# Performance work log

Measured on AMD Instinct MI355X. Metric: run time of the kernel, lower is better.

Reference implementation:

```python
import jax, jax.numpy as jnp
import numpy as np

C = 32          # mid_channel / in_channel
B = 8           # batch size (number of scenes)
N = 2_000_000   # total points across batch
BN_EPS = 1e-4   # BatchNorm1d eps from norm_fn


def setup_inputs() -> dict:
    key = jax.random.key(0)
    ks = jax.random.split(key, 8)
    s = 0.05
    return {
        "feats": jax.random.normal(ks[0], (N, C), dtype=jnp.float32),
        "batch_idxs": jnp.sort(jax.random.randint(ks[1], (N,), 0, B, dtype=jnp.int32)),
        "off_w1": jax.random.normal(ks[2], (C, C), dtype=jnp.float32) * s,
        "off_b1": jnp.zeros((C,), jnp.float32),
        "bn_gamma": jnp.ones((C,), jnp.float32),   # set_bn_init fills 1.0
        "bn_beta": jnp.zeros((C,), jnp.float32),   # set_bn_init fills 0.0
        "off_w2": jax.random.normal(ks[3], (C, 3), dtype=jnp.float32) * s,
        "off_b2": jnp.zeros((3,), jnp.float32),
        "mask_w1": jax.random.normal(ks[4], (C, C), dtype=jnp.float32) * s,
        "mask_b1": jnp.zeros((C,), jnp.float32),
        "mask_w2": jax.random.normal(ks[5], (C, 1), dtype=jnp.float32) * s,
        "mask_b2": jnp.zeros((1,), jnp.float32),
        "iou_w": jax.random.normal(ks[6], (C, 1), dtype=jnp.float32) * s,
        "iou_b": jnp.zeros((1,), jnp.float32),
    }


def reference(feats, batch_idxs, off_w1, off_b1, bn_gamma, bn_beta, off_w2, off_b2,
              mask_w1, mask_b1, mask_w2, mask_b2, iou_w, iou_b):
    # offset_linear = MLP([C, C, 3], norm_fn=BatchNorm1d): Linear -> BN -> ReLU -> Linear
    h = feats @ off_w1 + off_b1                      # [N, C]
    mu = h.mean(axis=0)
    var = jnp.mean(jnp.square(h - mu), axis=0)       # biased var (torch BN training fwd)
    h = (h - mu) * jax.lax.rsqrt(var + BN_EPS) * bn_gamma + bn_beta
    h = jax.nn.relu(h)
    pt_offsets = h @ off_w2 + off_b2                 # [N, 3]

    # mask_linear = MLP([C, C, 1], norm_fn=None): Linear -> ReLU -> Linear
    m = jax.nn.relu(feats @ mask_w1 + mask_b1)       # [N, C]
    mask_scores = m @ mask_w2 + mask_b2              # [N, 1]

    # global_pool: scatter mean of features over per-batch segments (batch offsets)
    ones = jnp.ones((feats.shape[0],), feats.dtype)
    counts = jax.ops.segment_sum(ones, batch_idxs, num_segments=B)          # [B]
    pooled = jax.ops.segment_sum(feats, batch_idxs, num_segments=B)         # [B, C]
    pooled = pooled / jnp.maximum(counts, 1.0)[:, None]

    # iou_score_linear on the pooled proposal feature
    iou_scores = pooled @ iou_w + iou_b              # [B, 1]
    return pt_offsets, mask_scores, pooled, iou_scores
```

## Files before the change

kernel.cpp:

```cpp
#include <hip/hip_runtime.h>

#define TPB 256
#define GRID_BLOCKS 1024

typedef __attribute__((ext_vector_type(8))) short short8;
typedef __attribute__((ext_vector_type(4))) float floatx4;

__device__ __forceinline__ unsigned short bf_rne(float f){
    union { float f; unsigned u; } c; c.f = f;
    unsigned r = c.u + 0x7fffu + ((c.u >> 16) & 1u);
    return (unsigned short)(r >> 16);
}
__device__ __forceinline__ unsigned pack_bf(float lo, float hi){
    union { float f; unsigned u; } a, b; a.f = lo; b.f = hi;
    return __builtin_amdgcn_perm(b.u, a.u, 0x07060302u);
}

__global__ __launch_bounds__(TPB, 2) void pass1_kernel(
    const float* __restrict__ feats, const int* __restrict__ bidx,
    const float* __restrict__ w1, const float* __restrict__ b1,
    const float* __restrict__ mw1, const float* __restrict__ mb1,
    const float* __restrict__ mw2, const float* __restrict__ mb2,
    float* __restrict__ mask_out,
    float* __restrict__ ws_sum, float* __restrict__ ws_sq,
    float* __restrict__ ws_pool, int N, int B)
{
    __shared__ float s_pool[8][32];
    __shared__ float s_sum[32];
    __shared__ float s_sq[32];
    __shared__ int   s_lb[9];

    const int tid  = threadIdx.x;
    const int lane = tid & 63;
    const int p = lane & 15;
    const int q = lane >> 4;

    if (tid < 32){ s_sum[tid] = 0.f; s_sq[tid] = 0.f; }
    ((float*)s_pool)[tid] = 0.f;
    if (tid <= B){
        int lo = 0, hi = N;
        while (lo < hi){
            const int mid = (lo + hi) >> 1;
            if (bidx[mid] < tid) lo = mid + 1; else hi = mid;
        }
        s_lb[tid] = lo;
    }
    __syncthreads();

    short8 aw0, aw1, am0, am1;
    floatx4 ci_h0, ci_h1, ci_m0, ci_m1;
    float mw2v[8];
#pragma unroll
    for (int j = 0; j < 8; ++j){
        const int k = q * 8 + j;
        aw0[j] = (short)bf_rne(w1 [k * 32 + p]);
        aw1[j] = (short)bf_rne(w1 [k * 32 + 16 + p]);
        am0[j] = (short)bf_rne(mw1[k * 32 + p]);
        am1[j] = (short)bf_rne(mw1[k * 32 + 16 + p]);
    }
#pragma unroll
    for (int r = 0; r < 4; ++r){
        const int c0 = q * 4 + r, c1 = 16 + q * 4 + r;
        ci_h0[r] = b1[c0];  ci_h1[r] = b1[c1];
        ci_m0[r] = mb1[c0]; ci_m1[r] = mb1[c1];
        mw2v[r] = mw2[c0];  mw2v[4 + r] = mw2[c1];
    }
    const float mb2s = mb2[0];

    float hsum[8] = {0,0,0,0,0,0,0,0};
    float hsq [8] = {0,0,0,0,0,0,0,0};
    float pacc[8] = {0,0,0,0,0,0,0,0};

    const int npairs = (N + 31) >> 5;
    const int nw  = gridDim.x * (TPB / 64);
    const int wid = blockIdx.x * (TPB / 64) + (tid >> 6);
    const int g0  = (int)((long)wid       * npairs / nw);
    const int g1  = (int)((long)(wid + 1) * npairs / nw);

    int curb = 0;
    {
        const int r0 = g0 << 5;
        while (curb < B - 1 && r0 >= s_lb[curb + 1]) curb++;
    }
    int lbn = s_lb[curb + 1];

    const float* rp = feats + (((size_t)g0) << 10) + (p << 5) + (q << 3);

    floatx4 vA0 = {0,0,0,0}, vA1 = {0,0,0,0}, vB0 = {0,0,0,0}, vB1 = {0,0,0,0};
    if (g0 < g1){
        const int rA = (g0 << 5) + p;
        if (rA < N){ const floatx4* vp = (const floatx4*)rp; vA0 = vp[0]; vA1 = vp[1]; }
        if (rA + 16 < N){ const floatx4* vp = (const floatx4*)(rp + 512); vB0 = vp[0]; vB1 = vp[1]; }
    }

    for (int g = g0; g < g1; ++g){
        floatx4 nA0 = {0,0,0,0}, nA1 = {0,0,0,0}, nB0 = {0,0,0,0}, nB1 = {0,0,0,0};
        const float* np = rp + 1024;
        if (g + 1 < g1){
            const int rA = ((g + 1) << 5) + p;
            if (rA < N){ const floatx4* vp = (const floatx4*)np; nA0 = vp[0]; nA1 = vp[1]; }
            if (rA + 16 < N){ const floatx4* vp = (const floatx4*)(np + 512); nB0 = vp[0]; nB1 = vp[1]; }
        }

        const int r0 = g << 5;
        if (r0 >= lbn){
#pragma unroll
            for (int j = 0; j < 8; ++j){
                if (pacc[j] != 0.f) atomicAdd(&s_pool[curb][q * 8 + j], pacc[j]);
                pacc[j] = 0.f;
            }
            do { curb++; } while (curb < B - 1 && r0 >= s_lb[curb + 1]);
            lbn = s_lb[curb + 1];
        }
        const bool slow = (r0 + 31 >= lbn) || (r0 + 31 >= N);

        if (!slow){
            pacc[0] += vA0[0] + vB0[0]; pacc[1] += vA0[1] + vB0[1];
            pacc[2] += vA0[2] + vB0[2]; pacc[3] += vA0[3] + vB0[3];
            pacc[4] += vA1[0] + vB1[0]; pacc[5] += vA1[1] + vB1[1];
            pacc[6] += vA1[2] + vB1[2]; pacc[7] += vA1[3] + vB1[3];
        } else {
            const int rA = r0 + p, rB = r0 + 16 + p;
            if (rA < N){
                int bl = curb;
                for (int c = curb + 1; c < B; ++c) bl += (rA >= s_lb[c]);
                atomicAdd(&s_pool[bl][q * 8 + 0], vA0[0]);
                atomicAdd(&s_pool[bl][q * 8 + 1], vA0[1]);
                atomicAdd(&s_pool[bl][q * 8 + 2], vA0[2]);
                atomicAdd(&s_pool[bl][q * 8 + 3], vA0[3]);
                atomicAdd(&s_pool[bl][q * 8 + 4], vA1[0]);
                atomicAdd(&s_pool[bl][q * 8 + 5], vA1[1]);
                atomicAdd(&s_pool[bl][q * 8 + 6], vA1[2]);
                atomicAdd(&s_pool[bl][q * 8 + 7], vA1[3]);
            }
            if (rB < N){
                int bl = curb;
                for (int c = curb + 1; c < B; ++c) bl += (rB >= s_lb[c]);
                atomicAdd(&s_pool[bl][q * 8 + 0], vB0[0]);
                atomicAdd(&s_pool[bl][q * 8 + 1], vB0[1]);
                atomicAdd(&s_pool[bl][q * 8 + 2], vB0[2]);
                atomicAdd(&s_pool[bl][q * 8 + 3], vB0[3]);
                atomicAdd(&s_pool[bl][q * 8 + 4], vB1[0]);
                atomicAdd(&s_pool[bl][q * 8 + 5], vB1[1]);
                atomicAdd(&s_pool[bl][q * 8 + 6], vB1[2]);
                atomicAdd(&s_pool[bl][q * 8 + 7], vB1[3]);
            }
        }

        short8 bfA, bfB;
        {
            unsigned* ba = (unsigned*)&bfA;
            ba[0] = pack_bf(vA0[0], vA0[1]); ba[1] = pack_bf(vA0[2], vA0[3]);
            ba[2] = pack_bf(vA1[0], vA1[1]); ba[3] = pack_bf(vA1[2], vA1[3]);
            unsigned* bb = (unsigned*)&bfB;
            bb[0] = pack_bf(vB0[0], vB0[1]); bb[1] = pack_bf(vB0[2], vB0[3]);
            bb[2] = pack_bf(vB1[0], vB1[1]); bb[3] = pack_bf(vB1[2], vB1[3]);
        }

        const floatx4 chA0 = __builtin_amdgcn_mfma_f32_16x16x32_bf16(aw0, bfA, ci_h0, 0, 0, 0);
        const floatx4 chA1 = __builtin_amdgcn_mfma_f32_16x16x32_bf16(aw1, bfA, ci_h1, 0, 0, 0);
        const floatx4 cmA0 = __builtin_amdgcn_mfma_f32_16x16x32_bf16(am0, bfA, ci_m0, 0, 0, 0);
        const floatx4 cmA1 = __builtin_amdgcn_mfma_f32_16x16x32_bf16(am1, bfA, ci_m1, 0, 0, 0);
        const floatx4 chB0 = __builtin_amdgcn_mfma_f32_16x16x32_bf16(aw0, bfB, ci_h0, 0, 0, 0);
        const floatx4 chB1 = __builtin_amdgcn_mfma_f32_16x16x32_bf16(aw1, bfB, ci_h1, 0, 0, 0);
        const floatx4 cmB0 = __builtin_amdgcn_mfma_f32_16x16x32_bf16(am0, bfB, ci_m0, 0, 0, 0);
        const floatx4 cmB1 = __builtin_amdgcn_mfma_f32_16x16x32_bf16(am1, bfB, ci_m1, 0, 0, 0);

        if (!slow){
#pragma unroll
            for (int r = 0; r < 4; ++r){
                const float a0 = chA0[r], b0 = chB0[r];
                hsum[r] += a0 + b0;
                hsq [r] = fmaf(a0, a0, fmaf(b0, b0, hsq[r]));
                const float a1 = chA1[r], b1v = chB1[r];
                hsum[4 + r] += a1 + b1v;
                hsq [4 + r] = fmaf(a1, a1, fmaf(b1v, b1v, hsq[4 + r]));
            }
        } else {
            if (r0 + p < N){
#pragma unroll
                for (int r = 0; r < 4; ++r){
                    const float a0 = chA0[r]; hsum[r]     += a0; hsq[r]     = fmaf(a0, a0, hsq[r]);
                    const float a1 = chA1[r]; hsum[4 + r] += a1; hsq[4 + r] = fmaf(a1, a1, hsq[4 + r]);
                }
            }
            if (r0 + 16 + p < N){
#pragma unroll
                for (int r = 0; r < 4; ++r){
                    const float b0 = chB0[r]; hsum[r]     += b0; hsq[r]     = fmaf(b0, b0, hsq[r]);
                    const float b1v = chB1[r]; hsum[4 + r] += b1v; hsq[4 + r] = fmaf(b1v, b1v, hsq[4 + r]);
                }
            }
        }

        float tmA = 0.f, tmB = 0.f;
#pragma unroll
        for (int r = 0; r < 4; ++r){
            tmA = fmaf(fmaxf(cmA0[r], 0.f), mw2v[r],     tmA);
            tmA = fmaf(fmaxf(cmA1[r], 0.f), mw2v[4 + r], tmA);
            tmB = fmaf(fmaxf(cmB0[r], 0.f), mw2v[r],     tmB);
            tmB = fmaf(fmaxf(cmB1[r], 0.f), mw2v[4 + r], tmB);
        }
        tmA += __shfl_xor(tmA, 16, 64); tmA += __shfl_xor(tmA, 32, 64);
        tmB += __shfl_xor(tmB, 16, 64); tmB += __shfl_xor(tmB, 32, 64);
        if (q == 0 && (r0 + p) < N)      mask_out[r0 + p]      = tmA + mb2s;
        if (q == 0 && (r0 + 16 + p) < N) mask_out[r0 + 16 + p] = tmB + mb2s;

        vA0 = nA0; vA1 = nA1; vB0 = nB0; vB1 = nB1; rp = np;
    }

#pragma unroll
    for (int j = 0; j < 8; ++j){
        if (pacc[j] != 0.f) atomicAdd(&s_pool[curb][q * 8 + j], pacc[j]);
    }
#pragma unroll
    for (int i = 0; i < 8; ++i){
        const int ch = (i >> 2) * 16 + q * 4 + (i & 3);
        atomicAdd(&s_sum[ch], hsum[i]);
        atomicAdd(&s_sq[ch],  hsq[i]);
    }
    __syncthreads();
    if (tid < 32){
        atomicAdd(&ws_sum[tid], s_sum[tid]);
        atomicAdd(&ws_sq[tid],  s_sq[tid]);
    }
    {
        const float pv = ((float*)s_pool)[tid];
        if (pv != 0.f) atomicAdd(&ws_pool[tid], pv);
    }
}

__global__ __launch_bounds__(TPB, 2) void pass2_kernel(
    const float* __restrict__ feats, const int* __restrict__ bidx,
    const float* __restrict__ w1, const float* __restrict__ b1,
    const float* __restrict__ gamma, const float* __restrict__ beta,
    const float* __restrict__ w2, const float* __restrict__ b2,
    const float* __restrict__ iw, const float* __restrict__ ib,
    const float* __restrict__ ws_sum, const float* __restrict__ ws_sq,
    const float* __restrict__ ws_pool,
    float* __restrict__ pt_out, float* __restrict__ pooled_out,
    float* __restrict__ iou_out, int N, int B)
{
    __shared__ float s_sc[32];
    __shared__ float s_bp[32];
    __shared__ float s_pooled[256];
    __shared__ int   s_lb[33];

    const int tid  = threadIdx.x;
    const int lane = tid & 63;
    const int p = lane & 15;
    const int q = lane >> 4;

    if (tid < 32){
        const float invN = 1.f / (float)N;
        const float mu  = ws_sum[tid] * invN;
        const float var = ws_sq[tid] * invN - mu * mu;
        const float s   = gamma[tid] * rsqrtf(var + 1e-4f);
        s_sc[tid] = s;
        s_bp[tid] = (b1[tid] - mu) * s + beta[tid];
    }
    __syncthreads();

    if (blockIdx.x == 0){
        if (tid <= B){
            int lo = 0, hi = N;
            while (lo < hi){
                const int mid = (lo + hi) >> 1;
                if (bidx[mid] < tid) lo = mid + 1; else hi = mid;
            }
            s_lb[tid] = lo;
        }
        __syncthreads();
        if (tid < B * 32){
            const int bb = tid >> 5;
            const float cnt = fmaxf((float)(s_lb[bb + 1] - s_lb[bb]), 1.f);
            const float pv = ws_pool[tid] / cnt;
            s_pooled[tid]   = pv;
            pooled_out[tid] = pv;
        }
        __syncthreads();
        if (tid < B){
            float acc = ib[0];
#pragma unroll
            for (int i = 0; i < 32; ++i) acc = fmaf(s_pooled[tid * 32 + i], iw[i], acc);
            iou_out[tid] = acc;
        }
    }

    short8 pw0, pw1;
    floatx4 pc0, pc1;
    float w2v[24];
    const float sc0 = s_sc[p], sc1 = s_sc[16 + p];
#pragma unroll
    for (int j = 0; j < 8; ++j){
        const int k = q * 8 + j;
        pw0[j] = (short)bf_rne(w1[k * 32 + p]      * sc0);
        pw1[j] = (short)bf_rne(w1[k * 32 + 16 + p] * sc1);
    }
#pragma unroll
    for (int r = 0; r < 4; ++r){
        pc0[r] = s_bp[q * 4 + r];
        pc1[r] = s_bp[16 + q * 4 + r];
    }
#pragma unroll
    for (int i = 0; i < 8; ++i){
        const int ch = (i >> 2) * 16 + q * 4 + (i & 3);
        w2v[i]      = w2[ch * 3 + 0];
        w2v[8 + i]  = w2[ch * 3 + 1];
        w2v[16 + i] = w2[ch * 3 + 2];
    }
    const float b2v0 = b2[0], b2v1 = b2[1], b2v2 = b2[2];

    const int npairs = (N + 31) >> 5;
    const int nw  = gridDim.x * (TPB / 64);
    const int wid = blockIdx.x * (TPB / 64) + (tid >> 6);
    const int g0  = (int)((long)wid       * npairs / nw);
    const int g1  = (int)((long)(wid + 1) * npairs / nw);

    const float* rp = feats + (((size_t)g0) << 10) + (p << 5) + (q << 3);

    floatx4 vA0 = {0,0,0,0}, vA1 = {0,0,0,0}, vB0 = {0,0,0,0}, vB1 = {0,0,0,0};
    if (g0 < g1){
        const int rA = (g0 << 5) + p;
        if (rA < N){ const floatx4* vp = (const floatx4*)rp; vA0 = vp[0]; vA1 = vp[1]; }
        if (rA + 16 < N){ const floatx4* vp = (const floatx4*)(rp + 512); vB0 = vp[0]; vB1 = vp[1]; }
    }

    for (int g = g0; g < g1; ++g){
        floatx4 nA0 = {0,0,0,0}, nA1 = {0,0,0,0}, nB0 = {0,0,0,0}, nB1 = {0,0,0,0};
        const float* np = rp + 1024;
        if (g + 1 < g1){
            const int rA = ((g + 1) << 5) + p;
            if (rA < N){ const floatx4* vp = (const floatx4*)np; nA0 = vp[0]; nA1 = vp[1]; }
            if (rA + 16 < N){ const floatx4* vp = (const floatx4*)(np + 512); nB0 = vp[0]; nB1 = vp[1]; }
        }

        short8 bfA, bfB;
        {
            unsigned* ba = (unsigned*)&bfA;
            ba[0] = pack_bf(vA0[0], vA0[1]); ba[1] = pack_bf(vA0[2], vA0[3]);
            ba[2] = pack_bf(vA1[0], vA1[1]); ba[3] = pack_bf(vA1[2], vA1[3]);
            unsigned* bb = (unsigned*)&bfB;
            bb[0] = pack_bf(vB0[0], vB0[1]); bb[1] = pack_bf(vB0[2], vB0[3]);
            bb[2] = pack_bf(vB1[0], vB1[1]); bb[3] = pack_bf(vB1[2], vB1[3]);
        }

        const floatx4 cA0 = __builtin_amdgcn_mfma_f32_16x16x32_bf16(pw0, bfA, pc0, 0, 0, 0);
        const floatx4 cA1 = __builtin_amdgcn_mfma_f32_16x16x32_bf16(pw1, bfA, pc1, 0, 0, 0);
        const floatx4 cB0 = __builtin_amdgcn_mfma_f32_16x16x32_bf16(pw0, bfB, pc0, 0, 0, 0);
        const floatx4 cB1 = __builtin_amdgcn_mfma_f32_16x16x32_bf16(pw1, bfB, pc1, 0, 0, 0);

        float sA0 = 0.f, sA1 = 0.f, sA2 = 0.f, sB0 = 0.f, sB1 = 0.f, sB2 = 0.f;
#pragma unroll
        for (int r = 0; r < 4; ++r){
            const float a0 = fmaxf(cA0[r], 0.f);
            const float a1 = fmaxf(cA1[r], 0.f);
            sA0 = fmaf(a0, w2v[r],      sA0); sA0 = fmaf(a1, w2v[4 + r],  sA0);
            sA1 = fmaf(a0, w2v[8 + r],  sA1); sA1 = fmaf(a1, w2v[12 + r], sA1);
            sA2 = fmaf(a0, w2v[16 + r], sA2); sA2 = fmaf(a1, w2v[20 + r], sA2);
            const float b0 = fmaxf(cB0[r], 0.f);
            const float b1v = fmaxf(cB1[r], 0.f);
            sB0 = fmaf(b0, w2v[r],      sB0); sB0 = fmaf(b1v, w2v[4 + r],  sB0);
            sB1 = fmaf(b0, w2v[8 + r],  sB1); sB1 = fmaf(b1v, w2v[12 + r], sB1);
            sB2 = fmaf(b0, w2v[16 + r], sB2); sB2 = fmaf(b1v, w2v[20 + r], sB2);
        }
        sA0 += __shfl_xor(sA0, 16, 64); sA0 += __shfl_xor(sA0, 32, 64);
        sA1 += __shfl_xor(sA1, 16, 64); sA1 += __shfl_xor(sA1, 32, 64);
        sA2 += __shfl_xor(sA2, 16, 64); sA2 += __shfl_xor(sA2, 32, 64);
        sB0 += __shfl_xor(sB0, 16, 64); sB0 += __shfl_xor(sB0, 32, 64);
        sB1 += __shfl_xor(sB1, 16, 64); sB1 += __shfl_xor(sB1, 32, 64);
        sB2 += __shfl_xor(sB2, 16, 64); sB2 += __shfl_xor(sB2, 32, 64);

        const int r0 = g << 5;
        const int rA = r0 + p, rB = r0 + 16 + p;
        if (lane < 48 && rA < N){
            float val = (q == 0) ? (sA0 + b2v0) : ((q == 1) ? (sA1 + b2v1) : (sA2 + b2v2));
            pt_out[(size_t)rA * 3 + q] = val;
        }
        if (lane < 48 && rB < N){
            float val = (q == 0) ? (sB0 + b2v0) : ((q == 1) ? (sB1 + b2v1) : (sB2 + b2v2));
            pt_out[(size_t)rB * 3 + q] = val;
        }

        vA0 = nA0; vA1 = nA1; vB0 = nB0; vB1 = nB1; rp = np;
    }
}

extern "C" void kernel_launch(void* const* d_in, const int* in_sizes, int n_in,
                              void* d_out, int out_size, void* d_ws, size_t ws_size,
                              hipStream_t stream) {
    const float* feats = (const float*)d_in[0];
    const int*   bidx  = (const int*)d_in[1];
    const float* w1    = (const float*)d_in[2];
    const float* b1    = (const float*)d_in[3];
    const float* gamma = (const float*)d_in[4];
    const float* beta  = (const float*)d_in[5];
    const float* w2    = (const float*)d_in[6];
    const float* b2    = (const float*)d_in[7];
    const float* mw1   = (const float*)d_in[8];
    const float* mb1   = (const float*)d_in[9];
    const float* mw2   = (const float*)d_in[10];
    const float* mb2   = (const float*)d_in[11];
    const float* iw    = (const float*)d_in[12];
    const float* ib    = (const float*)d_in[13];

    const int N = in_sizes[0] / 32;
    const int B = (out_size - 4 * N) / 33;

    float* out    = (float*)d_out;
    float* pt     = out;
    float* mask   = out + (size_t)3 * N;
    float* pooled = out + (size_t)4 * N;
    float* iou    = pooled + (size_t)B * 32;

    float* ws      = (float*)d_ws;
    float* ws_sum  = ws;
    float* ws_sq   = ws + 32;
    float* ws_pool = ws + 64;

    hipMemsetAsync(ws, 0, (size_t)(64 + B * 32) * sizeof(float), stream);

    pass1_kernel<<<GRID_BLOCKS, TPB, 0, stream>>>(feats, bidx, w1, b1, mw1, mb1, mw2, mb2,
                                                  mask, ws_sum, ws_sq, ws_pool, N, B);
    pass2_kernel<<<GRID_BLOCKS, TPB, 0, stream>>>(feats, bidx, w1, b1, gamma, beta, w2, b2,
                                                  iw, ib, ws_sum, ws_sq, ws_pool,
                                                  pt, pooled, iou, N, B);
}
```

Before: 480.9 us.

## Stage feature loads through swizzled LDS and hoist segment bounds into a kernel

Global loads of feats now go fully coalesced (each lane reads consecutive float4s across rows) into a per-wave XOR-swizzled LDS tile, then get re-read in the MFMA operand layout. The old per-lane strided row loads are gone. The binary search for batch boundaries moves into a tiny separate kernel whose results both passes read. The grid is sized from occupancy queries instead of a fixed 1024 blocks. In exchange this adds LDS traffic, an extra launch, and host-side device-property queries on every call.

```diff
diff --git a/kernel.cpp b/kernel.cpp
--- a/kernel.cpp
+++ b/kernel.cpp
@@ -1,7 +1,6 @@
 #include <hip/hip_runtime.h>
 
 #define TPB 256
-#define GRID_BLOCKS 1024
 
 typedef __attribute__((ext_vector_type(8))) short short8;
 typedef __attribute__((ext_vector_type(4))) float floatx4;
@@ -16,8 +15,22 @@
     return __builtin_amdgcn_perm(b.u, a.u, 0x07060302u);
 }
 
-__global__ __launch_bounds__(TPB, 2) void pass1_kernel(
-    const float* __restrict__ feats, const int* __restrict__ bidx,
+__global__ void lb_kernel(const int* __restrict__ bidx, int* __restrict__ ws_lb,
+                          int N, int B)
+{
+    const int t = threadIdx.x;
+    if (t <= B){
+        int lo = 0, hi = N;
+        while (lo < hi){
+            const int mid = (lo + hi) >> 1;
+            if (bidx[mid] < t) lo = mid + 1; else hi = mid;
+        }
+        ws_lb[t] = lo;
+    }
+}
+
+__global__ __launch_bounds__(TPB) void pass1_kernel(
+    const float* __restrict__ feats, const int* __restrict__ ws_lb,
     const float* __restrict__ w1, const float* __restrict__ b1,
     const float* __restrict__ mw1, const float* __restrict__ mb1,
     const float* __restrict__ mw2, const float* __restrict__ mb2,
@@ -25,6 +38,7 @@
     float* __restrict__ ws_sum, float* __restrict__ ws_sq,
     float* __restrict__ ws_pool, int N, int B)
 {
+    __shared__ float s_stage[TPB/64][1024];
     __shared__ float s_pool[8][32];
     __shared__ float s_sum[32];
     __shared__ float s_sq[32];
@@ -32,19 +46,13 @@
 
     const int tid  = threadIdx.x;
     const int lane = tid & 63;
+    const int wv   = tid >> 6;
     const int p = lane & 15;
     const int q = lane >> 4;
 
     if (tid < 32){ s_sum[tid] = 0.f; s_sq[tid] = 0.f; }
     ((float*)s_pool)[tid] = 0.f;
-    if (tid <= B){
-        int lo = 0, hi = N;
-        while (lo < hi){
-            const int mid = (lo + hi) >> 1;
-            if (bidx[mid] < tid) lo = mid + 1; else hi = mid;
-        }
-        s_lb[tid] = lo;
-    }
+    if (tid <= B) s_lb[tid] = ws_lb[tid];
     __syncthreads();
 
     short8 aw0, aw1, am0, am1;
@@ -69,44 +77,77 @@
 
     float hsum[8] = {0,0,0,0,0,0,0,0};
     float hsq [8] = {0,0,0,0,0,0,0,0};
-    float pacc[8] = {0,0,0,0,0,0,0,0};
-
-    const int npairs = (N + 31) >> 5;
+    float pacc[4] = {0,0,0,0};
+
+    const int ngroups = (N + 31) >> 5;
     const int nw  = gridDim.x * (TPB / 64);
-    const int wid = blockIdx.x * (TPB / 64) + (tid >> 6);
-    const int g0  = (int)((long)wid       * npairs / nw);
-    const int g1  = (int)((long)(wid + 1) * npairs / nw);
+    const int wid = blockIdx.x * (TPB / 64) + wv;
+    const int g0  = (int)((long)wid       * ngroups / nw);
+    const int gE  = (int)((long)(wid + 1) * ngroups / nw);
 
     int curb = 0;
-    {
-        const int r0 = g0 << 5;
-        while (curb < B - 1 && r0 >= s_lb[curb + 1]) curb++;
-    }
+    { const int r = g0 << 5; while (curb < B - 1 && r >= s_lb[curb + 1]) curb++; }
     int lbn = s_lb[curb + 1];
 
-    const float* rp = feats + (((size_t)g0) << 10) + (p << 5) + (q << 3);
-
-    floatx4 vA0 = {0,0,0,0}, vA1 = {0,0,0,0}, vB0 = {0,0,0,0}, vB1 = {0,0,0,0};
-    if (g0 < g1){
-        const int rA = (g0 << 5) + p;
-        if (rA < N){ const floatx4* vp = (const floatx4*)rp; vA0 = vp[0]; vA1 = vp[1]; }
-        if (rA + 16 < N){ const floatx4* vp = (const floatx4*)(rp + 512); vB0 = vp[0]; vB1 = vp[1]; }
-    }
-
-    for (int g = g0; g < g1; ++g){
-        floatx4 nA0 = {0,0,0,0}, nA1 = {0,0,0,0}, nB0 = {0,0,0,0}, nB1 = {0,0,0,0};
-        const float* np = rp + 1024;
-        if (g + 1 < g1){
-            const int rA = ((g + 1) << 5) + p;
-            if (rA < N){ const floatx4* vp = (const floatx4*)np; nA0 = vp[0]; nA1 = vp[1]; }
-            if (rA + 16 < N){ const floatx4* vp = (const floatx4*)(np + 512); nB0 = vp[0]; nB1 = vp[1]; }
+    float* sw = &s_stage[wv][0];
+    const int wrow  = lane >> 3;
+    const int wg    = (lane & 7) ^ wrow;
+    const int cbase = (lane & 7) << 2;
+    const int wo0 = ( 0 + wrow) * 32 + (wg << 2);
+    const int wo1 = ( 8 + wrow) * 32 + (wg << 2);
+    const int wo2 = (16 + wrow) * 32 + (wg << 2);
+    const int wo3 = (24 + wrow) * 32 + (wg << 2);
+    const int e = p & 7;
+    const int ra0 = p * 32        + ((((q << 1)    ) ^ e) << 2);
+    const int ra1 = p * 32        + ((((q << 1) + 1) ^ e) << 2);
+    const int rb0 = (16 + p) * 32 + ((((q << 1)    ) ^ e) << 2);
+    const int rb1 = (16 + p) * 32 + ((((q << 1) + 1) ^ e) << 2);
+
+    floatx4 sv0 = {0,0,0,0}, sv1 = {0,0,0,0}, sv2 = {0,0,0,0}, sv3 = {0,0,0,0};
+    if (g0 < gE){
+        const float* gp = feats + ((size_t)g0 << 10) + (lane << 2);
+        const int r = (g0 << 5) + wrow;
+        if (r + 24 < N){
+            sv0 = *(const floatx4*)(gp);
+            sv1 = *(const floatx4*)(gp + 256);
+            sv2 = *(const floatx4*)(gp + 512);
+            sv3 = *(const floatx4*)(gp + 768);
+        } else {
+            if (r      < N) sv0 = *(const floatx4*)(gp);
+            if (r +  8 < N) sv1 = *(const floatx4*)(gp + 256);
+            if (r + 16 < N) sv2 = *(const floatx4*)(gp + 512);
+            if (r + 24 < N) sv3 = *(const floatx4*)(gp + 768);
+        }
+    }
+
+    for (int g = g0; g < gE; ++g){
+        *(floatx4*)(sw + wo0) = sv0;
+        *(floatx4*)(sw + wo1) = sv1;
+        *(floatx4*)(sw + wo2) = sv2;
+        *(floatx4*)(sw + wo3) = sv3;
+
+        floatx4 nv0 = {0,0,0,0}, nv1 = {0,0,0,0}, nv2 = {0,0,0,0}, nv3 = {0,0,0,0};
+        if (g + 1 < gE){
+            const float* gp = feats + ((size_t)(g + 1) << 10) + (lane << 2);
+            const int r = ((g + 1) << 5) + wrow;
+            if (r + 24 < N){
+                nv0 = *(const floatx4*)(gp);
+                nv1 = *(const floatx4*)(gp + 256);
+                nv2 = *(const floatx4*)(gp + 512);
+                nv3 = *(const floatx4*)(gp + 768);
+            } else {
+                if (r      < N) nv0 = *(const floatx4*)(gp);
+                if (r +  8 < N) nv1 = *(const floatx4*)(gp + 256);
+                if (r + 16 < N) nv2 = *(const floatx4*)(gp + 512);
+                if (r + 24 < N) nv3 = *(const floatx4*)(gp + 768);
+            }
         }
 
         const int r0 = g << 5;
         if (r0 >= lbn){
 #pragma unroll
-            for (int j = 0; j < 8; ++j){
-                if (pacc[j] != 0.f) atomicAdd(&s_pool[curb][q * 8 + j], pacc[j]);
+            for (int j = 0; j < 4; ++j){
+                if (pacc[j] != 0.f) atomicAdd(&s_pool[curb][cbase + j], pacc[j]);
                 pacc[j] = 0.f;
             }
             do { curb++; } while (curb < B - 1 && r0 >= s_lb[curb + 1]);
@@ -115,37 +156,29 @@
         const bool slow = (r0 + 31 >= lbn) || (r0 + 31 >= N);
 
         if (!slow){
-            pacc[0] += vA0[0] + vB0[0]; pacc[1] += vA0[1] + vB0[1];
-            pacc[2] += vA0[2] + vB0[2]; pacc[3] += vA0[3] + vB0[3];
-            pacc[4] += vA1[0] + vB1[0]; pacc[5] += vA1[1] + vB1[1];
-            pacc[6] += vA1[2] + vB1[2]; pacc[7] += vA1[3] + vB1[3];
+            pacc[0] += sv0[0] + sv1[0] + sv2[0] + sv3[0];
+            pacc[1] += sv0[1] + sv1[1] + sv2[1] + sv3[1];
+            pacc[2] += sv0[2] + sv1[2] + sv2[2] + sv3[2];
+            pacc[3] += sv0[3] + sv1[3] + sv2[3] + sv3[3];
         } else {
-            const int rA = r0 + p, rB = r0 + 16 + p;
-            if (rA < N){
-                int bl = curb;
-                for (int c = curb + 1; c < B; ++c) bl += (rA >= s_lb[c]);
-                atomicAdd(&s_pool[bl][q * 8 + 0], vA0[0]);
-                atomicAdd(&s_pool[bl][q * 8 + 1], vA0[1]);
-                atomicAdd(&s_pool[bl][q * 8 + 2], vA0[2]);
-                atomicAdd(&s_pool[bl][q * 8 + 3], vA0[3]);
-                atomicAdd(&s_pool[bl][q * 8 + 4], vA1[0]);
-                atomicAdd(&s_pool[bl][q * 8 + 5], vA1[1]);
-                atomicAdd(&s_pool[bl][q * 8 + 6], vA1[2]);
-                atomicAdd(&s_pool[bl][q * 8 + 7], vA1[3]);
-            }
-            if (rB < N){
-                int bl = curb;
-                for (int c = curb + 1; c < B; ++c) bl += (rB >= s_lb[c]);
-                atomicAdd(&s_pool[bl][q * 8 + 0], vB0[0]);
-                atomicAdd(&s_pool[bl][q * 8 + 1], vB0[1]);
-                atomicAdd(&s_pool[bl][q * 8 + 2], vB0[2]);
-                atomicAdd(&s_pool[bl][q * 8 + 3], vB0[3]);
-                atomicAdd(&s_pool[bl][q * 8 + 4], vB1[0]);
-                atomicAdd(&s_pool[bl][q * 8 + 5], vB1[1]);
-                atomicAdd(&s_pool[bl][q * 8 + 6], vB1[2]);
-                atomicAdd(&s_pool[bl][q * 8 + 7], vB1[3]);
-            }
-        }
+#define SLOWROW(SV, L) { \
+            const int row = r0 + (L * 8) + wrow; \
+            if (row < N){ \
+                int bl = curb; \
+                for (int c = curb + 1; c < B; ++c) bl += (row >= s_lb[c]); \
+                atomicAdd(&s_pool[bl][cbase + 0], SV[0]); \
+                atomicAdd(&s_pool[bl][cbase + 1], SV[1]); \
+                atomicAdd(&s_pool[bl][cbase + 2], SV[2]); \
+                atomicAdd(&s_pool[bl][cbase + 3], SV[3]); \
+            } }
+            SLOWROW(sv0, 0) SLOWROW(sv1, 1) SLOWROW(sv2, 2) SLOWROW(sv3, 3)
+#undef SLOWROW
+        }
+
+        const floatx4 vA0 = *(const floatx4*)(sw + ra0);
+        const floatx4 vA1 = *(const floatx4*)(sw + ra1);
+        const floatx4 vB0 = *(const floatx4*)(sw + rb0);
+        const floatx4 vB1 = *(const floatx4*)(sw + rb1);
 
         short8 bfA, bfB;
         {
@@ -166,7 +199,7 @@
         const floatx4 cmB0 = __builtin_amdgcn_mfma_f32_16x16x32_bf16(am0, bfB, ci_m0, 0, 0, 0);
         const floatx4 cmB1 = __builtin_amdgcn_mfma_f32_16x16x32_bf16(am1, bfB, ci_m1, 0, 0, 0);
 
-        if (!slow){
+        if (r0 + 31 < N){
 #pragma unroll
             for (int r = 0; r < 4; ++r){
                 const float a0 = chA0[r], b0 = chB0[r];
@@ -206,12 +239,12 @@
         if (q == 0 && (r0 + p) < N)      mask_out[r0 + p]      = tmA + mb2s;
         if (q == 0 && (r0 + 16 + p) < N) mask_out[r0 + 16 + p] = tmB + mb2s;
 
-        vA0 = nA0; vA1 = nA1; vB0 = nB0; vB1 = nB1; rp = np;
-    }
-
-#pragma unroll
-    for (int j = 0; j < 8; ++j){
-        if (pacc[j] != 0.f) atomicAdd(&s_pool[curb][q * 8 + j], pacc[j]);
+        sv0 = nv0; sv1 = nv1; sv2 = nv2; sv3 = nv3;
+    }
+
+#pragma unroll
+    for (int j = 0; j < 4; ++j){
+        if (pacc[j] != 0.f) atomicAdd(&s_pool[curb][cbase + j], pacc[j]);
     }
 #pragma unroll
     for (int i = 0; i < 8; ++i){
@@ -230,8 +263,8 @@
     }
 }
 
-__global__ __launch_bounds__(TPB, 2) void pass2_kernel(
-    const float* __restrict__ feats, const int* __restrict__ bidx,
+__global__ __launch_bounds__(TPB) void pass2_kernel(
+    const float* __restrict__ feats, const int* __restrict__ ws_lb,
     const float* __restrict__ w1, const float* __restrict__ b1,
     const float* __restrict__ gamma, const float* __restrict__ beta,
     const float* __restrict__ w2, const float* __restrict__ b2,
@@ -241,13 +274,15 @@
     float* __restrict__ pt_out, float* __restrict__ pooled_out,
     float* __restrict__ iou_out, int N, int B)
 {
+    __shared__ float s_stage[TPB/64][1024];
     __shared__ float s_sc[32];
     __shared__ float s_bp[32];
     __shared__ float s_pooled[256];
-    __shared__ int   s_lb[33];
+    __shared__ int   s_lb[9];
 
     const int tid  = threadIdx.x;
     const int lane = tid & 63;
+    const int wv   = tid >> 6;
     const int p = lane & 15;
     const int q = lane >> 4;
 
@@ -259,18 +294,10 @@
         s_sc[tid] = s;
         s_bp[tid] = (b1[tid] - mu) * s + beta[tid];
     }
+    if (tid <= B) s_lb[tid] = ws_lb[tid];
     __syncthreads();
 
     if (blockIdx.x == 0){
-        if (tid <= B){
-            int lo = 0, hi = N;
-            while (lo < hi){
-                const int mid = (lo + hi) >> 1;
-                if (bidx[mid] < tid) lo = mid + 1; else hi = mid;
-            }
-            s_lb[tid] = lo;
-        }
-        __syncthreads();
         if (tid < B * 32){
             const int bb = tid >> 5;
             const float cnt = fmaxf((float)(s_lb[bb + 1] - s_lb[bb]), 1.f);
@@ -311,29 +338,69 @@
     }
     const float b2v0 = b2[0], b2v1 = b2[1], b2v2 = b2[2];
 
-    const int npairs = (N + 31) >> 5;
+    const int ngroups = (N + 31) >> 5;
     const int nw  = gridDim.x * (TPB / 64);
-    const int wid = blockIdx.x * (TPB / 64) + (tid >> 6);
-    const int g0  = (int)((long)wid       * npairs / nw);
-    const int g1  = (int)((long)(wid + 1) * npairs / nw);
-
-    const float* rp = feats + (((size_t)g0) << 10) + (p << 5) + (q << 3);
-
-    floatx4 vA0 = {0,0,0,0}, vA1 = {0,0,0,0}, vB0 = {0,0,0,0}, vB1 = {0,0,0,0};
-    if (g0 < g1){
-        const int rA = (g0 << 5) + p;
-        if (rA < N){ const floatx4* vp = (const floatx4*)rp; vA0 = vp[0]; vA1 = vp[1]; }
-        if (rA + 16 < N){ const floatx4* vp = (const floatx4*)(rp + 512); vB0 = vp[0]; vB1 = vp[1]; }
-    }
-
-    for (int g = g0; g < g1; ++g){
-        floatx4 nA0 = {0,0,0,0}, nA1 = {0,0,0,0}, nB0 = {0,0,0,0}, nB1 = {0,0,0,0};
-        const float* np = rp + 1024;
-        if (g + 1 < g1){
-            const int rA = ((g + 1) << 5) + p;
-            if (rA < N){ const floatx4* vp = (const floatx4*)np; nA0 = vp[0]; nA1 = vp[1]; }
-            if (rA + 16 < N){ const floatx4* vp = (const floatx4*)(np + 512); nB0 = vp[0]; nB1 = vp[1]; }
-        }
+    const int wid = blockIdx.x * (TPB / 64) + wv;
+    const int g0  = (int)((long)wid       * ngroups / nw);
+    const int gE  = (int)((long)(wid + 1) * ngroups / nw);
+
+    float* sw = &s_stage[wv][0];
+    const int wrow = lane >> 3;
+    const int wg   = (lane & 7) ^ wrow;
+    const int wo0 = ( 0 + wrow) * 32 + (wg << 2);
+    const int wo1 = ( 8 + wrow) * 32 + (wg << 2);
+    const int wo2 = (16 + wrow) * 32 + (wg << 2);
+    const int wo3 = (24 + wrow) * 32 + (wg << 2);
+    const int e = p & 7;
+    const int ra0 = p * 32        + ((((q << 1)    ) ^ e) << 2);
+    const int ra1 = p * 32        + ((((q << 1) + 1) ^ e) << 2);
+    const int rb0 = (16 + p) * 32 + ((((q << 1)    ) ^ e) << 2);
+    const int rb1 = (16 + p) * 32 + ((((q << 1) + 1) ^ e) << 2);
+
+    floatx4 sv0 = {0,0,0,0}, sv1 = {0,0,0,0}, sv2 = {0,0,0,0}, sv3 = {0,0,0,0};
+    if (g0 < gE){
+        const float* gp = feats + ((size_t)g0 << 10) + (lane << 2);
+        const int r = (g0 << 5) + wrow;
+        if (r + 24 < N){
+            sv0 = *(const floatx4*)(gp);
+            sv1 = *(const floatx4*)(gp + 256);
+            sv2 = *(const floatx4*)(gp + 512);
+            sv3 = *(const floatx4*)(gp + 768);
+        } else {
+            if (r      < N) sv0 = *(const floatx4*)(gp);
+            if (r +  8 < N) sv1 = *(const floatx4*)(gp + 256);
+            if (r + 16 < N) sv2 = *(const floatx4*)(gp + 512);
+            if (r + 24 < N) sv3 = *(const floatx4*)(gp + 768);
+        }
+    }
+
+    for (int g = g0; g < gE; ++g){
+        *(floatx4*)(sw + wo0) = sv0;
+        *(floatx4*)(sw + wo1) = sv1;
+        *(floatx4*)(sw + wo2) = sv2;
+        *(floatx4*)(sw + wo3) = sv3;
+
+        floatx4 nv0 = {0,0,0,0}, nv1 = {0,0,0,0}, nv2 = {0,0,0,0}, nv3 = {0,0,0,0};
+        if (g + 1 < gE){
+            const float* gp = feats + ((size_t)(g + 1) << 10) + (lane << 2);
+            const int r = ((g + 1) << 5) + wrow;
+            if (r + 24 < N){
+                nv0 = *(const floatx4*)(gp);
+                nv1 = *(const floatx4*)(gp + 256);
+                nv2 = *(const floatx4*)(gp + 512);
+                nv3 = *(const floatx4*)(gp + 768);
+            } else {
+                if (r      < N) nv0 = *(const floatx4*)(gp);
+                if (r +  8 < N) nv1 = *(const floatx4*)(gp + 256);
+                if (r + 16 < N) nv2 = *(const floatx4*)(gp + 512);
+                if (r + 24 < N) nv3 = *(const floatx4*)(gp + 768);
+            }
+        }
+
+        const floatx4 vA0 = *(const floatx4*)(sw + ra0);
+        const floatx4 vA1 = *(const floatx4*)(sw + ra1);
+        const floatx4 vB0 = *(const floatx4*)(sw + rb0);
+        const floatx4 vB1 = *(const floatx4*)(sw + rb1);
 
         short8 bfA, bfB;
         {
@@ -382,7 +449,7 @@
             pt_out[(size_t)rB * 3 + q] = val;
         }
 
-        vA0 = nA0; vA1 = nA1; vB0 = nB0; vB1 = nB1; rp = np;
+        sv0 = nv0; sv1 = nv1; sv2 = nv2; sv3 = nv3;
     }
 }
 
@@ -417,12 +484,24 @@
     float* ws_sum  = ws;
     float* ws_sq   = ws + 32;
     float* ws_pool = ws + 64;
+    int*   ws_lb   = (int*)(ws + 64 + (size_t)B * 32);
 
     hipMemsetAsync(ws, 0, (size_t)(64 + B * 32) * sizeof(float), stream);
 
-    pass1_kernel<<<GRID_BLOCKS, TPB, 0, stream>>>(feats, bidx, w1, b1, mw1, mb1, mw2, mb2,
-                                                  mask, ws_sum, ws_sq, ws_pool, N, B);
-    pass2_kernel<<<GRID_BLOCKS, TPB, 0, stream>>>(feats, bidx, w1, b1, gamma, beta, w2, b2,
-                                                  iw, ib, ws_sum, ws_sq, ws_pool,
-                                                  pt, pooled, iou, N, B);
+    int dev = 0;
+    hipGetDevice(&dev);
+    hipDeviceProp_t prop;
+    hipGetDeviceProperties(&prop, dev);
+    int per1 = 0, per2 = 0;
+    hipOccupancyMaxActiveBlocksPerMultiprocessor(&per1, pass1_kernel, TPB, 0);
+    hipOccupancyMaxActiveBlocksPerMultiprocessor(&per2, pass2_kernel, TPB, 0);
+    int g1 = per1 * prop.multiProcessorCount; if (g1 < 512) g1 = 512;
+    int g2 = per2 * prop.multiProcessorCount; if (g2 < 512) g2 = 512;
+
+    lb_kernel<<<1, 64, 0, stream>>>(bidx, ws_lb, N, B);
+    pass1_kernel<<<g1, TPB, 0, stream>>>(feats, ws_lb, w1, b1, mw1, mb1, mw2, mb2,
+                                         mask, ws_sum, ws_sq, ws_pool, N, B);
+    pass2_kernel<<<g2, TPB, 0, stream>>>(feats, ws_lb, w1, b1, gamma, beta, w2, b2,
+                                         iw, ib, ws_sum, ws_sq, ws_pool,
+                                         pt, pooled, iou, N, B);
 }
```

Result: faster. 455.3 us (-5.3%).
